# Optimization experiments

Measured on AMD Instinct MI355X. Metric: run time of the kernel, lower is better.

The kernel has to match this reference:

```python
import jax, jax.numpy as jnp
import numpy as np

T, N, E = 12, 20000, 320000
FIN, H, G, C = 128, 256, 256, 10


def setup_inputs() -> dict:
    key = jax.random.key(0)
    ks = jax.random.split(key, 14)
    x = jax.random.normal(ks[0], (T, N, FIN), dtype=jnp.float32)
    edge_index = jax.random.randint(ks[1], (T, 2, E), 0, N)
    edge_attr = jax.random.uniform(ks[2], (T, E), dtype=jnp.float32)

    def lin(k, fan_in, shape):
        return jax.random.normal(k, shape, dtype=jnp.float32) / np.sqrt(fan_in).astype(np.float32)

    return {
        "x": x,
        "edge_index": edge_index,
        "edge_attr": edge_attr,
        "W1": lin(ks[3], FIN, (FIN, H)),
        "b1": jnp.zeros((H,), jnp.float32),
        "W2": lin(ks[4], H, (H, H)),
        "b2": jnp.zeros((H,), jnp.float32),
        "Wih": lin(ks[5], H, (3 * G, H)),
        "Whh": lin(ks[6], G, (3 * G, G)),
        "bih": jnp.zeros((3 * G,), jnp.float32),
        "bhh": jnp.zeros((3 * G,), jnp.float32),
        "Wc": lin(ks[7], G, (G, C)),
        "bc": jnp.zeros((C,), jnp.float32),
    }


def _gcn_conv(h, row, col, w, W, b):
    # PyG GCNConv: h' = D^{-1/2} (A + I) D^{-1/2} (h W) + b, with edge weights w
    h = h @ W  # [N, H]
    deg = jax.ops.segment_sum(w, col, num_segments=N) + 1.0  # self-loop weight 1
    dinv = jax.lax.rsqrt(deg)  # [N]
    norm = dinv[row] * w * dinv[col]  # [E]
    agg = jax.ops.segment_sum(norm[:, None] * h[row], col, num_segments=N)
    agg = agg + (dinv * dinv)[:, None] * h  # self-loop contribution
    return agg + b


def reference(x, edge_index, edge_attr, W1, b1, W2, b2, Wih, Whh, bih, bhh, Wc, bc):
    def snapshot(carry, inp):
        xs, ei, ea = inp
        row, col = ei[0], ei[1]
        h = jax.nn.relu(_gcn_conv(xs, row, col, ea, W1, b1))
        h = jax.nn.relu(_gcn_conv(h, row, col, ea, W2, b2))
        return carry, h.mean(axis=0)  # mean pool over nodes -> [H]

    _, embs = jax.lax.scan(snapshot, 0, (x, edge_index, edge_attr))  # [T, H]

    def gru_step(hprev, xt):
        gx = Wih @ xt + bih  # [3G]
        gh = Whh @ hprev + bhh
        r = jax.nn.sigmoid(gx[:G] + gh[:G])
        z = jax.nn.sigmoid(gx[G:2 * G] + gh[G:2 * G])
        n = jnp.tanh(gx[2 * G:] + r * gh[2 * G:])
        hnew = (1.0 - z) * n + z * hprev
        return hnew, None

    last_h, _ = jax.lax.scan(gru_step, jnp.zeros((G,), x.dtype), embs)
    out = last_h @ Wc + bc  # [C]
    return out[None, :]  # [1, num_classes]
```

## Files before the change

### kernel.cpp

```cpp
#include <hip/hip_runtime.h>
#include <hip/hip_fp16.h>
#include <math.h>

#define T_ 12
#define N_ 20000
#define E_ 320000
#define FIN_ 128
#define H_ 256
#define G_ 256
#define C_ 10
#define ECH 8
#define EPC (E_ / ECH)
#define NB 20
#define BNODES 1024
#define CAPF 18432

typedef __attribute__((ext_vector_type(8))) short bf16x8;
typedef __attribute__((ext_vector_type(4))) float f32x4;

static const size_t OFF_EMB   = 0;
static const size_t ZERO_BYTES= 12288;
static const size_t OFF_DINV  = 12288;
static const size_t OFF_CP    = 972288;
static const size_t OFF_DEGP  = 1932544;
static const size_t OFF_CNT16 = 9612544;
static const size_t OFF_EBIN  = 1932544;
static const size_t OFF_PCNT  = 32652544;
static const size_t OFF_POFF  = 32660224;
static const size_t OFF_EREC  = 32668288;
static const size_t OFF_W1BT  = 48028288;
static const size_t OFF_W2BT  = 48093824;
static const size_t OFF_WIHT  = 48224896;
static const size_t OFF_WHHT  = 49011328;
static const size_t OFF_GX    = 49797760;
static const size_t OFF_RA    = 49834624;
static const size_t PER_T_FULL= 10240000;

__device__ __forceinline__ float bf2f(unsigned short u) {
  return __uint_as_float(((unsigned int)u) << 16);
}
__device__ __forceinline__ unsigned short f2bf(float f) {
  unsigned int u = __float_as_uint(f);
  unsigned int r = (u + 0x7FFFu + ((u >> 16) & 1u)) >> 16;
  return (unsigned short)r;
}
__device__ __forceinline__ float bflo(unsigned int u) { return __uint_as_float(u << 16); }
__device__ __forceinline__ float bfhi(unsigned int u) { return __uint_as_float(u & 0xFFFF0000u); }
__device__ __forceinline__ unsigned int packbf(float lo, float hi) {
  return (unsigned int)f2bf(lo) | ((unsigned int)f2bf(hi) << 16);
}
__device__ __forceinline__ float rec2nm(unsigned int rec) {
  return __half2float(__ushort_as_half((unsigned short)(rec >> 16)));
}

__global__ __launch_bounds__(1024) void histp(const int* __restrict__ ei,
                                              const float* __restrict__ ea,
                                              float* __restrict__ degp,
                                              unsigned short* __restrict__ cnt16) {
  __shared__ float degs[N_];
  __shared__ unsigned int cntp[N_ / 2];
  const int t = blockIdx.x, ech = blockIdx.y;
  const int tid = threadIdx.x;
  for (int i = tid; i < N_; i += 1024) degs[i] = 0.f;
  for (int i = tid; i < N_ / 2; i += 1024) cntp[i] = 0u;
  __syncthreads();
  const int* col = ei + (size_t)t * 2 * E_ + E_ + ech * EPC;
  const float* wt = ea + (size_t)t * E_ + ech * EPC;
  for (int e = tid; e < EPC; e += 1024) {
    int c = col[e];
    atomicAdd(&degs[c], wt[e]);
    atomicAdd(&cntp[c >> 1], 1u << ((c & 1) * 16));
  }
  __syncthreads();
  float* dp = degp + ((size_t)t * ECH + ech) * N_;
  unsigned short* cp16 = cnt16 + ((size_t)t * ECH + ech) * N_;
  for (int i = tid; i < N_; i += 1024) {
    dp[i] = degs[i];
    cp16[i] = (unsigned short)((cntp[i >> 1] >> ((i & 1) * 16)) & 0xFFFFu);
  }
}

__global__ __launch_bounds__(1024) void scanT(const unsigned short* __restrict__ cnt16,
                                              const float* __restrict__ degp,
                                              int* __restrict__ colptr,
                                              float* __restrict__ dinv) {
  const int t = blockIdx.x;
  __shared__ int s[1024];
  const int tid = threadIdx.x;
  int base = 0;
  for (int c0 = 0; c0 < N_; c0 += 1024) {
    int n = c0 + tid;
    int tot = 0;
    float dg = 0.f;
    if (n < N_) {
#pragma unroll
      for (int ch = 0; ch < ECH; ++ch) {
        tot += cnt16[((size_t)t * ECH + ch) * N_ + n];
        dg += degp[((size_t)t * ECH + ch) * N_ + n];
      }
    }
    s[tid] = tot;
    __syncthreads();
    for (int off = 1; off < 1024; off <<= 1) {
      int add = (tid >= off) ? s[tid - off] : 0;
      __syncthreads();
      s[tid] += add;
      __syncthreads();
    }
    if (n < N_) {
      colptr[t * (N_ + 1) + n] = base + s[tid] - tot;
      dinv[t * N_ + n] = rsqrtf(dg + 1.0f);
    }
    base += s[1023];
    __syncthreads();
  }
  if (tid == 0) colptr[t * (N_ + 1) + N_] = base;
}

__global__ __launch_bounds__(256) void pcount(const unsigned short* __restrict__ cnt16,
                                              unsigned int* __restrict__ pcnt) {
  __shared__ unsigned int psum[NB];
  const int t = blockIdx.x, ech = blockIdx.y;
  const int tid = threadIdx.x;
  if (tid < NB) psum[tid] = 0u;
  __syncthreads();
  const unsigned short* cc = cnt16 + ((size_t)t * ECH + ech) * N_;
  for (int c0 = 0; c0 < N_; c0 += 256) {
    int n = c0 + tid;
    unsigned int v = (n < N_) ? (unsigned int)cc[n] : 0u;
#pragma unroll
    for (int off = 32; off; off >>= 1) v += __shfl_down(v, off, 64);
    if ((tid & 63) == 0) atomicAdd(&psum[c0 >> 10], v);
  }
  __syncthreads();
  if (tid < NB) pcnt[((size_t)t * ECH + ech) * NB + tid] = psum[tid];
}

__global__ void partS(const unsigned int* __restrict__ pcnt,
                      unsigned int* __restrict__ poff) {
  const int t = threadIdx.x;
  if (t >= T_) return;
  unsigned int run = 0;
  for (int b = 0; b < NB; ++b)
    for (int ech = 0; ech < ECH; ++ech) {
      poff[t * 168 + b * 8 + ech] = run;
      run += pcnt[((size_t)t * ECH + ech) * NB + b];
    }
  poff[t * 168 + 160] = run;
}

__global__ __launch_bounds__(512) void partW(const int* __restrict__ ei,
                                             const float* __restrict__ ea,
                                             const float* __restrict__ dinv,
                                             const unsigned int* __restrict__ poff,
                                             uint2* __restrict__ ebin) {
  __shared__ unsigned int cursor[NB];
  const int t = blockIdx.x, ech = blockIdx.y;
  const int tid = threadIdx.x;
  if (tid < NB) cursor[tid] = poff[t * 168 + tid * 8 + ech];
  __syncthreads();
  const int eoff = ech * EPC;
  const int* rowp = ei + (size_t)t * 2 * E_ + eoff;
  const int* colp = rowp + E_;
  const float* wt = ea + (size_t)t * E_ + eoff;
  const float* dv = dinv + (size_t)t * N_;
  uint2* eb = ebin + (size_t)t * E_;
  for (int e = tid; e < EPC; e += 512) {
    int c = colp[e], r = rowp[e];
    float nm = dv[r] * wt[e] * dv[c];
    unsigned int pos = atomicAdd(&cursor[c >> 10], 1u);
    uint2 rec;
    rec.x = (unsigned int)(c & 1023) | ((unsigned int)r << 16);
    rec.y = (unsigned int)__half_as_ushort(__float2half(nm));
    eb[pos] = rec;
  }
}

__global__ __launch_bounds__(512) void fillB2(const uint2* __restrict__ ebin,
                                              const int* __restrict__ colptr,
                                              unsigned int* __restrict__ erec) {
  __shared__ unsigned int data[CAPF];
  __shared__ unsigned int offp[BNODES];
  const int t = blockIdx.x, b = blockIdx.y;
  const int tid = threadIdx.x;
  const int nlo = b << 10;
  const int nnodes = (N_ - nlo < BNODES) ? (N_ - nlo) : BNODES;
  const int* cp = colptr + t * (N_ + 1);
  const int base = cp[nlo];
  const int bsize = cp[nlo + nnodes] - base;
  for (int i = tid; i < nnodes; i += 512) offp[i] = (unsigned int)(cp[nlo + i] - base);
  __syncthreads();
  const uint2* eb = ebin + (size_t)t * E_ + base;
  unsigned int* eg = erec + (size_t)t * E_ + base;
  for (int i = tid; i < bsize; i += 512) {
    uint2 rec = eb[i];
    unsigned int cl = rec.x & 0xFFFFu;
    unsigned int rec4 = (rec.x >> 16) | (rec.y << 16);
    unsigned int pos = atomicAdd(&offp[cl], 1u);
    if (pos < CAPF) data[pos] = rec4;
    else eg[pos] = rec4;
  }
  __syncthreads();
  const int lim = bsize < CAPF ? bsize : CAPF;
  for (int i = tid; i < lim; i += 512) eg[i] = data[i];
}

__global__ __launch_bounds__(256) void prep_kernel(const float* __restrict__ W1,
                                                   const float* __restrict__ W2,
                                                   const float* __restrict__ Wih,
                                                   const float* __restrict__ Whh,
                                                   unsigned short* __restrict__ W1bT,
                                                   unsigned short* __restrict__ W2bT,
                                                   float* __restrict__ WihT,
                                                   float* __restrict__ WhhT) {
  int idx = blockIdx.x * 256 + threadIdx.x;
  if (idx < 32768) {
    int n = idx >> 7, k = idx & 127;
    W1bT[idx] = f2bf(W1[k * 256 + n]);
  } else if (idx < 98304) {
    int j = idx - 32768;
    int n = j >> 8, k = j & 255;
    W2bT[j] = f2bf(W2[k * 256 + n]);
  } else if (idx < 294912) {
    int j = idx - 98304;
    int k = j / 768, c = j - k * 768;
    WihT[j] = Wih[c * 256 + k];
  } else if (idx < 491520) {
    int j = idx - 294912;
    int k = j / 768, c = j - k * 768;
    WhhT[j] = Whh[c * 256 + k];
  }
}

__global__ __launch_bounds__(256) void castx_kernel(const float* __restrict__ x,
                                                    unsigned short* __restrict__ xb,
                                                    int t_base) {
  const int tl = blockIdx.y;
  const int t = t_base + tl;
  const size_t q = (size_t)blockIdx.x * 256 + threadIdx.x;
  float4 v = ((const float4*)x)[(size_t)t * (N_ * FIN_ / 4) + q];
  ushort4 o;
  o.x = f2bf(v.x); o.y = f2bf(v.y); o.z = f2bf(v.z); o.w = f2bf(v.w);
  ((ushort4*)xb)[(size_t)tl * (N_ * FIN_ / 4) + q] = o;
}

template <int CHN, int NPASS>
__global__ __launch_bounds__(256) void aggP(const unsigned short* __restrict__ h,
                                            unsigned short* __restrict__ o,
                                            const unsigned int* __restrict__ erec,
                                            const int* __restrict__ colptr,
                                            const float* __restrict__ dinv,
                                            int t_base, int nt) {
  int bid = blockIdx.x;
  int L = bid;
  if (nt > 1) {
    int chunk = (int)(gridDim.x >> 3);
    L = (bid & 7) * chunk + (bid >> 3);
  }
  const int PT = NPASS * 5000;
  const int tl = L / PT;
  int rem = L - tl * PT;
  const int pass = rem / 5000;
  const int nb = rem - pass * 5000;
  const int node = nb * 4 + ((int)threadIdx.x >> 6);
  const int t = t_base + tl;
  const int g = ((int)threadIdx.x >> 3) & 7;
  const int j = threadIdx.x & 7;
  const int me = threadIdx.x & 63;
  const unsigned int* ert = erec + (size_t)t * E_;
  const int* cp = colptr + t * (N_ + 1);
  const unsigned short* ht = h + (size_t)tl * N_ * CHN + pass * 64;
  float a0 = 0.f, a1 = 0.f, a2 = 0.f, a3 = 0.f, a4 = 0.f, a5 = 0.f, a6 = 0.f, a7 = 0.f;
  const int s0 = cp[node], s1 = cp[node + 1];
  for (int i = s0 + g; i < s1; i += 8) {
    const unsigned int rec = ert[i];
    const int r = rec & 0xFFFFu;
    const float nm = rec2nm(rec);
    uint4 u = *(const uint4*)&ht[(size_t)r * CHN + j * 8];
    a0 = fmaf(nm, bflo(u.x), a0); a1 = fmaf(nm, bfhi(u.x), a1);
    a2 = fmaf(nm, bflo(u.y), a2); a3 = fmaf(nm, bfhi(u.y), a3);
    a4 = fmaf(nm, bflo(u.z), a4); a5 = fmaf(nm, bfhi(u.z), a5);
    a6 = fmaf(nm, bflo(u.w), a6); a7 = fmaf(nm, bfhi(u.w), a7);
  }
  if (g == 0) {
    const float di = dinv[(size_t)t * N_ + node];
    const float sw = di * di;
    uint4 us = *(const uint4*)&ht[(size_t)node * CHN + j * 8];
    a0 = fmaf(sw, bflo(us.x), a0); a1 = fmaf(sw, bfhi(us.x), a1);
    a2 = fmaf(sw, bflo(us.y), a2); a3 = fmaf(sw, bfhi(us.y), a3);
    a4 = fmaf(sw, bflo(us.z), a4); a5 = fmaf(sw, bfhi(us.z), a5);
    a6 = fmaf(sw, bflo(us.w), a6); a7 = fmaf(sw, bfhi(us.w), a7);
  }
#pragma unroll
  for (int off = 8; off <= 32; off <<= 1) {
    a0 += __shfl(a0, me ^ off, 64); a1 += __shfl(a1, me ^ off, 64);
    a2 += __shfl(a2, me ^ off, 64); a3 += __shfl(a3, me ^ off, 64);
    a4 += __shfl(a4, me ^ off, 64); a5 += __shfl(a5, me ^ off, 64);
    a6 += __shfl(a6, me ^ off, 64); a7 += __shfl(a7, me ^ off, 64);
  }
  if (g == 0) {
    uint4 ov;
    ov.x = packbf(a0, a1); ov.y = packbf(a2, a3);
    ov.z = packbf(a4, a5); ov.w = packbf(a6, a7);
    unsigned short* ot = o + (size_t)tl * N_ * CHN + pass * 64;
    *(uint4*)&ot[(size_t)node * CHN + j * 8] = ov;
  }
}

template <int K, bool MEAN>
__global__ __launch_bounds__(256) void gemm_bf16(const unsigned short* __restrict__ A,
                                                 const unsigned short* __restrict__ BT,
                                                 const float* __restrict__ bias,
                                                 unsigned short* __restrict__ C,
                                                 float* __restrict__ embp,
                                                 int t_base) {
  constexpr int LD = K + 8;
  __shared__ unsigned short As[64 * LD];
  __shared__ float cs[128];
  const int tid = threadIdx.x;
  const int tl = blockIdx.z;
  const int bm = blockIdx.x * 64;
  const int bn = blockIdx.y * 128;
  const unsigned short* At = A + (size_t)tl * N_ * K;
  if (MEAN && tid < 128) cs[tid] = 0.f;
  {
    constexpr int CPR = K / 8;
    constexpr int CH = 64 * CPR / 256;
#pragma unroll
    for (int i = 0; i < CH; ++i) {
      int chunk = tid + i * 256;
      int r = chunk / CPR;
      int ck = (chunk - r * CPR) * 8;
      int row = bm + r;
      if (row >= N_) row = N_ - 1;
      *(bf16x8*)&As[r * LD + ck] = *(const bf16x8*)&At[(size_t)row * K + ck];
    }
  }
  __syncthreads();
  const int w = tid >> 6, l = tid & 63;
  const int l16 = l & 15, lk = l >> 4;
  const int rbase = (w >> 1) * 32;
  const int colbase = bn + (w & 1) * 64;
  f32x4 acc[2][4] = {};
  for (int ks = 0; ks < K; ks += 32) {
    bf16x8 a[2], b[4];
#pragma unroll
    for (int m = 0; m < 2; ++m)
      a[m] = *(const bf16x8*)&As[(rbase + m * 16 + l16) * LD + ks + lk * 8];
#pragma unroll
    for (int n = 0; n < 4; ++n)
      b[n] = *(const bf16x8*)&BT[(size_t)(colbase + n * 16 + l16) * K + ks + lk * 8];
#pragma unroll
    for (int m = 0; m < 2; ++m)
#pragma unroll
      for (int n = 0; n < 4; ++n)
        acc[m][n] = __builtin_amdgcn_mfma_f32_16x16x32_bf16(a[m], b[n], acc[m][n], 0, 0, 0);
  }
#pragma unroll
  for (int n = 0; n < 4; ++n) {
    int col = colbase + n * 16 + l16;
    float bv = bias[col];
    float psum = 0.f;
#pragma unroll
    for (int m = 0; m < 2; ++m) {
      int row0 = bm + rbase + m * 16 + lk * 4;
#pragma unroll
      for (int r = 0; r < 4; ++r) {
        int row = row0 + r;
        if (row < N_) {
          float v = fmaxf(acc[m][n][r] + bv, 0.f);
          if (MEAN) psum += v;
          else C[((size_t)tl * N_ + row) * 256 + col] = f2bf(v);
        }
      }
    }
    if (MEAN) atomicAdd(&cs[col - bn], psum);
  }
  if (MEAN) {
    __syncthreads();
    if (tid < 128)
      atomicAdd(&embp[(t_base + tl) * 256 + bn + tid], cs[tid] * (1.0f / N_));
  }
}

__global__ __launch_bounds__(768) void gx_kernel(const float* __restrict__ emb,
                                                 const float* __restrict__ WihT,
                                                 const float* __restrict__ bih,
                                                 float* __restrict__ GX) {
  const int t = blockIdx.x;
  const int tid = threadIdx.x;
  __shared__ float se[256];
  if (tid < 256) se[tid] = emb[t * 256 + tid];
  __syncthreads();
  float p0 = 0.f, p1 = 0.f, p2 = 0.f, p3 = 0.f;
#pragma unroll 8
  for (int k = 0; k < 256; k += 4) {
    p0 = fmaf(WihT[(size_t)(k + 0) * 768 + tid], se[k + 0], p0);
    p1 = fmaf(WihT[(size_t)(k + 1) * 768 + tid], se[k + 1], p1);
    p2 = fmaf(WihT[(size_t)(k + 2) * 768 + tid], se[k + 2], p2);
    p3 = fmaf(WihT[(size_t)(k + 3) * 768 + tid], se[k + 3], p3);
  }
  GX[t * 768 + tid] = (p0 + p1) + (p2 + p3) + bih[tid];
}

__global__ __launch_bounds__(768) void gru2_kernel(const float* __restrict__ GX,
                                                   const float* __restrict__ WhhT,
                                                   const float* __restrict__ bhh,
                                                   const float* __restrict__ Wc,
                                                   const float* __restrict__ bc,
                                                   float* __restrict__ out) {
  __shared__ float sh[256];
  __shared__ float sgh[768];
  const int tid = threadIdx.x;
  if (tid < 256) sh[tid] = 0.f;
  __syncthreads();
  for (int t = 0; t < T_; ++t) {
    float p0 = 0.f, p1 = 0.f, p2 = 0.f, p3 = 0.f;
#pragma unroll 8
    for (int k = 0; k < 256; k += 4) {
      p0 = fmaf(WhhT[(size_t)(k + 0) * 768 + tid], sh[k + 0], p0);
      p1 = fmaf(WhhT[(size_t)(k + 1) * 768 + tid], sh[k + 1], p1);
      p2 = fmaf(WhhT[(size_t)(k + 2) * 768 + tid], sh[k + 2], p2);
      p3 = fmaf(WhhT[(size_t)(k + 3) * 768 + tid], sh[k + 3], p3);
    }
    sgh[tid] = (p0 + p1) + (p2 + p3) + bhh[tid];
    __syncthreads();
    if (tid < 256) {
      const float* gx = &GX[t * 768];
      float r = 1.f / (1.f + __expf(-(gx[tid] + sgh[tid])));
      float z = 1.f / (1.f + __expf(-(gx[256 + tid] + sgh[256 + tid])));
      float n = tanhf(gx[512 + tid] + r * sgh[512 + tid]);
      sh[tid] = (1.f - z) * n + z * sh[tid];
    }
    __syncthreads();
  }
  const int wv = tid >> 6, lane = tid & 63;
  if (wv < C_) {
    float p = 0.f;
#pragma unroll
    for (int i = 0; i < 4; ++i) {
      int j = lane + 64 * i;
      p += sh[j] * Wc[(size_t)j * C_ + wv];
    }
    for (int off = 32; off > 0; off >>= 1) p += __shfl_down(p, off);
    if (lane == 0) out[wv] = p + bc[wv];
  }
}

extern "C" void kernel_launch(void* const* d_in, const int* in_sizes, int n_in,
                              void* d_out, int out_size, void* d_ws, size_t ws_size,
                              hipStream_t stream) {
  const float* x   = (const float*)d_in[0];
  const int*   ei  = (const int*)d_in[1];
  const float* ea  = (const float*)d_in[2];
  const float* W1  = (const float*)d_in[3];
  const float* b1  = (const float*)d_in[4];
  const float* W2  = (const float*)d_in[5];
  const float* b2  = (const float*)d_in[6];
  const float* Wih = (const float*)d_in[7];
  const float* Whh = (const float*)d_in[8];
  const float* bih = (const float*)d_in[9];
  const float* bhh = (const float*)d_in[10];
  const float* Wc  = (const float*)d_in[11];
  const float* bc  = (const float*)d_in[12];
  float* out = (float*)d_out;

  char* w = (char*)d_ws;
  float* emb   = (float*)(w + OFF_EMB);
  float* dinv  = (float*)(w + OFF_DINV);
  int*   cp    = (int*)(w + OFF_CP);
  float* degp  = (float*)(w + OFF_DEGP);
  unsigned short* cnt16 = (unsigned short*)(w + OFF_CNT16);
  uint2* ebin  = (uint2*)(w + OFF_EBIN);
  unsigned int* pcnt = (unsigned int*)(w + OFF_PCNT);
  unsigned int* poff = (unsigned int*)(w + OFF_POFF);
  unsigned int* erec = (unsigned int*)(w + OFF_EREC);
  unsigned short* W1bT = (unsigned short*)(w + OFF_W1BT);
  unsigned short* W2bT = (unsigned short*)(w + OFF_W2BT);
  float* WihT  = (float*)(w + OFF_WIHT);
  float* WhhT  = (float*)(w + OFF_WHHT);
  float* GX    = (float*)(w + OFF_GX);

  int NT = 1;
  if (ws_size > OFF_RA + 2 * PER_T_FULL) {
    size_t avail = ws_size - OFF_RA;
    size_t nt = avail / (2 * PER_T_FULL);
    NT = (int)(nt < 12 ? nt : 12);
    if (NT < 1) NT = 1;
  }
  unsigned short* regA = (unsigned short*)(w + OFF_RA);
  unsigned short* regB = (unsigned short*)(w + OFF_RA + (size_t)NT * PER_T_FULL);
  unsigned short* xbt  = regA;
  unsigned short* Q    = regA;
  unsigned short* P128 = regB;
  unsigned short* P2   = regB;

  hipMemsetAsync(d_ws, 0, ZERO_BYTES, stream);

  prep_kernel<<<1920, 256, 0, stream>>>(W1, W2, Wih, Whh, W1bT, W2bT, WihT, WhhT);

  dim3 te_grid(T_, ECH);
  histp<<<te_grid, 1024, 0, stream>>>(ei, ea, degp, cnt16);
  scanT<<<T_, 1024, 0, stream>>>(cnt16, degp, cp, dinv);
  pcount<<<te_grid, 256, 0, stream>>>(cnt16, pcnt);
  partS<<<1, 64, 0, stream>>>(pcnt, poff);
  partW<<<te_grid, 512, 0, stream>>>(ei, ea, dinv, poff, ebin);
  fillB2<<<dim3(T_, NB), 512, 0, stream>>>(ebin, cp, erec);

  for (int t0 = 0; t0 < T_; t0 += NT) {
    const int nt = (T_ - t0) < NT ? (T_ - t0) : NT;
    castx_kernel<<<dim3(2500, nt), 256, 0, stream>>>(x, xbt, t0);
    aggP<128, 2><<<nt * 10000, 256, 0, stream>>>(xbt, P128, erec, cp, dinv, t0, nt);
    gemm_bf16<FIN_, false><<<dim3(313, 2, nt), 256, 0, stream>>>(P128, W1bT, b1, Q, nullptr, t0);
    aggP<256, 4><<<nt * 20000, 256, 0, stream>>>(Q, P2, erec, cp, dinv, t0, nt);
    gemm_bf16<H_, true><<<dim3(313, 2, nt), 256, 0, stream>>>(P2, W2bT, b2, nullptr, emb, t0);
  }
  gx_kernel<<<T_, 768, 0, stream>>>(emb, WihT, bih, GX);
  gru2_kernel<<<1, 768, 0, stream>>>(GX, WhhT, bhh, Wc, bc, out);
}
```

Baseline: 1.197 ms.

## Widen edge records to fp32 in place and remap aggregation lanes

fillB2 now writes node-sorted edge records back into the ebin buffer as uint2 pairs of row index and fp32 norm, replacing the separate packed erec array with its fp16 norm. The aggregation kernel is restructured so each wavefront covers 128 channels per pass, 4 channels per lane, with two lane halves splitting the edges. This halves the number of passes and replaces the three-step cross-lane reduction with a single shuffle. The cost is less memory-level parallelism per node, since each half-wave walks about half the edges in sequence, and twice the record bytes. The global overflow path for bins larger than CAPF is removed and only partly offset by raising CAPF, so an oversized bin would silently drop edges.

Result: slower. 1.283 ms (+7.2%).

```diff
diff --git a/kernel.cpp b/kernel.cpp
--- a/kernel.cpp
+++ b/kernel.cpp
@@ -13,7 +13,7 @@
 #define EPC (E_ / ECH)
 #define NB 20
 #define BNODES 1024
-#define CAPF 18432
+#define CAPF 20480
 
 typedef __attribute__((ext_vector_type(8))) short bf16x8;
 typedef __attribute__((ext_vector_type(4))) float f32x4;
@@ -27,7 +27,6 @@
 static const size_t OFF_EBIN  = 1932544;
 static const size_t OFF_PCNT  = 32652544;
 static const size_t OFF_POFF  = 32660224;
-static const size_t OFF_EREC  = 32668288;
 static const size_t OFF_W1BT  = 48028288;
 static const size_t OFF_W2BT  = 48093824;
 static const size_t OFF_WIHT  = 48224896;
@@ -48,9 +47,6 @@
 __device__ __forceinline__ float bfhi(unsigned int u) { return __uint_as_float(u & 0xFFFF0000u); }
 __device__ __forceinline__ unsigned int packbf(float lo, float hi) {
   return (unsigned int)f2bf(lo) | ((unsigned int)f2bf(hi) << 16);
-}
-__device__ __forceinline__ float rec2nm(unsigned int rec) {
-  return __half2float(__ushort_as_half((unsigned short)(rec >> 16)));
 }
 
 __global__ __launch_bounds__(1024) void histp(const int* __restrict__ ei,
@@ -176,9 +172,8 @@
   }
 }
 
-__global__ __launch_bounds__(512) void fillB2(const uint2* __restrict__ ebin,
-                                              const int* __restrict__ colptr,
-                                              unsigned int* __restrict__ erec) {
+__global__ __launch_bounds__(512) void fillB2(uint2* __restrict__ ebin,
+                                              const int* __restrict__ colptr) {
   __shared__ unsigned int data[CAPF];
   __shared__ unsigned int offp[BNODES];
   const int t = blockIdx.x, b = blockIdx.y;
@@ -190,19 +185,23 @@
   const int bsize = cp[nlo + nnodes] - base;
   for (int i = tid; i < nnodes; i += 512) offp[i] = (unsigned int)(cp[nlo + i] - base);
   __syncthreads();
-  const uint2* eb = ebin + (size_t)t * E_ + base;
-  unsigned int* eg = erec + (size_t)t * E_ + base;
+  uint2* eb = ebin + (size_t)t * E_ + base;
   for (int i = tid; i < bsize; i += 512) {
     uint2 rec = eb[i];
     unsigned int cl = rec.x & 0xFFFFu;
     unsigned int rec4 = (rec.x >> 16) | (rec.y << 16);
     unsigned int pos = atomicAdd(&offp[cl], 1u);
     if (pos < CAPF) data[pos] = rec4;
-    else eg[pos] = rec4;
   }
   __syncthreads();
   const int lim = bsize < CAPF ? bsize : CAPF;
-  for (int i = tid; i < lim; i += 512) eg[i] = data[i];
+  for (int i = tid; i < lim; i += 512) {
+    unsigned int rec4 = data[i];
+    uint2 o;
+    o.x = rec4 & 0xFFFFu;
+    o.y = __float_as_uint(__half2float(__ushort_as_half((unsigned short)(rec4 >> 16))));
+    eb[i] = o;
+  }
 }
 
 __global__ __launch_bounds__(256) void prep_kernel(const float* __restrict__ W1,
@@ -245,9 +244,9 @@
 }
 
 template <int CHN, int NPASS>
-__global__ __launch_bounds__(256) void aggP(const unsigned short* __restrict__ h,
+__global__ __launch_bounds__(256) void aggD(const unsigned short* __restrict__ h,
                                             unsigned short* __restrict__ o,
-                                            const unsigned int* __restrict__ erec,
+                                            const uint2* __restrict__ erec2,
                                             const int* __restrict__ colptr,
                                             const float* __restrict__ dinv,
                                             int t_base, int nt) {
@@ -264,46 +263,35 @@
   const int nb = rem - pass * 5000;
   const int node = nb * 4 + ((int)threadIdx.x >> 6);
   const int t = t_base + tl;
-  const int g = ((int)threadIdx.x >> 3) & 7;
-  const int j = threadIdx.x & 7;
+  const int hh = ((int)threadIdx.x >> 5) & 1;
+  const int l32 = threadIdx.x & 31;
   const int me = threadIdx.x & 63;
-  const unsigned int* ert = erec + (size_t)t * E_;
+  const uint2* ert = erec2 + (size_t)t * E_;
   const int* cp = colptr + t * (N_ + 1);
-  const unsigned short* ht = h + (size_t)tl * N_ * CHN + pass * 64;
-  float a0 = 0.f, a1 = 0.f, a2 = 0.f, a3 = 0.f, a4 = 0.f, a5 = 0.f, a6 = 0.f, a7 = 0.f;
+  const unsigned short* ht = h + (size_t)tl * N_ * CHN + pass * 128 + l32 * 4;
+  float a0 = 0.f, a1 = 0.f, a2 = 0.f, a3 = 0.f;
   const int s0 = cp[node], s1 = cp[node + 1];
-  for (int i = s0 + g; i < s1; i += 8) {
-    const unsigned int rec = ert[i];
-    const int r = rec & 0xFFFFu;
-    const float nm = rec2nm(rec);
-    uint4 u = *(const uint4*)&ht[(size_t)r * CHN + j * 8];
+  for (int i = s0 + hh; i < s1; i += 2) {
+    const uint2 rec = ert[i];
+    const float nm = __uint_as_float(rec.y);
+    uint2 u = *(const uint2*)&ht[(size_t)rec.x * CHN];
     a0 = fmaf(nm, bflo(u.x), a0); a1 = fmaf(nm, bfhi(u.x), a1);
     a2 = fmaf(nm, bflo(u.y), a2); a3 = fmaf(nm, bfhi(u.y), a3);
-    a4 = fmaf(nm, bflo(u.z), a4); a5 = fmaf(nm, bfhi(u.z), a5);
-    a6 = fmaf(nm, bflo(u.w), a6); a7 = fmaf(nm, bfhi(u.w), a7);
-  }
-  if (g == 0) {
+  }
+  if (hh == 0) {
     const float di = dinv[(size_t)t * N_ + node];
     const float sw = di * di;
-    uint4 us = *(const uint4*)&ht[(size_t)node * CHN + j * 8];
+    uint2 us = *(const uint2*)&ht[(size_t)node * CHN];
     a0 = fmaf(sw, bflo(us.x), a0); a1 = fmaf(sw, bfhi(us.x), a1);
     a2 = fmaf(sw, bflo(us.y), a2); a3 = fmaf(sw, bfhi(us.y), a3);
-    a4 = fmaf(sw, bflo(us.z), a4); a5 = fmaf(sw, bfhi(us.z), a5);
-    a6 = fmaf(sw, bflo(us.w), a6); a7 = fmaf(sw, bfhi(us.w), a7);
-  }
-#pragma unroll
-  for (int off = 8; off <= 32; off <<= 1) {
-    a0 += __shfl(a0, me ^ off, 64); a1 += __shfl(a1, me ^ off, 64);
-    a2 += __shfl(a2, me ^ off, 64); a3 += __shfl(a3, me ^ off, 64);
-    a4 += __shfl(a4, me ^ off, 64); a5 += __shfl(a5, me ^ off, 64);
-    a6 += __shfl(a6, me ^ off, 64); a7 += __shfl(a7, me ^ off, 64);
-  }
-  if (g == 0) {
-    uint4 ov;
+  }
+  a0 += __shfl(a0, me ^ 32, 64); a1 += __shfl(a1, me ^ 32, 64);
+  a2 += __shfl(a2, me ^ 32, 64); a3 += __shfl(a3, me ^ 32, 64);
+  if (hh == 0) {
+    uint2 ov;
     ov.x = packbf(a0, a1); ov.y = packbf(a2, a3);
-    ov.z = packbf(a4, a5); ov.w = packbf(a6, a7);
-    unsigned short* ot = o + (size_t)tl * N_ * CHN + pass * 64;
-    *(uint4*)&ot[(size_t)node * CHN + j * 8] = ov;
+    unsigned short* ot = o + (size_t)tl * N_ * CHN + pass * 128 + l32 * 4;
+    *(uint2*)&ot[(size_t)node * CHN] = ov;
   }
 }
 
@@ -474,7 +462,6 @@
   uint2* ebin  = (uint2*)(w + OFF_EBIN);
   unsigned int* pcnt = (unsigned int*)(w + OFF_PCNT);
   unsigned int* poff = (unsigned int*)(w + OFF_POFF);
-  unsigned int* erec = (unsigned int*)(w + OFF_EREC);
   unsigned short* W1bT = (unsigned short*)(w + OFF_W1BT);
   unsigned short* W2bT = (unsigned short*)(w + OFF_W2BT);
   float* WihT  = (float*)(w + OFF_WIHT);
@@ -505,14 +492,14 @@
   pcount<<<te_grid, 256, 0, stream>>>(cnt16, pcnt);
   partS<<<1, 64, 0, stream>>>(pcnt, poff);
   partW<<<te_grid, 512, 0, stream>>>(ei, ea, dinv, poff, ebin);
-  fillB2<<<dim3(T_, NB), 512, 0, stream>>>(ebin, cp, erec);
+  fillB2<<<dim3(T_, NB), 512, 0, stream>>>(ebin, cp);
 
   for (int t0 = 0; t0 < T_; t0 += NT) {
     const int nt = (T_ - t0) < NT ? (T_ - t0) : NT;
     castx_kernel<<<dim3(2500, nt), 256, 0, stream>>>(x, xbt, t0);
-    aggP<128, 2><<<nt * 10000, 256, 0, stream>>>(xbt, P128, erec, cp, dinv, t0, nt);
+    aggD<128, 1><<<nt * 5000, 256, 0, stream>>>(xbt, P128, (const uint2*)ebin, cp, dinv, t0, nt);
     gemm_bf16<FIN_, false><<<dim3(313, 2, nt), 256, 0, stream>>>(P128, W1bT, b1, Q, nullptr, t0);
-    aggP<256, 4><<<nt * 20000, 256, 0, stream>>>(Q, P2, erec, cp, dinv, t0, nt);
+    aggD<256, 2><<<nt * 10000, 256, 0, stream>>>(Q, P2, (const uint2*)ebin, cp, dinv, t0, nt);
     gemm_bf16<H_, true><<<dim3(313, 2, nt), 256, 0, stream>>>(P2, W2bT, b2, nullptr, emb, t0);
   }
   gx_kernel<<<T_, 768, 0, stream>>>(emb, WihT, bih, GX);
```
